# Optimization experiments

Hardware: AMD Instinct MI355X
Metric: run time of the kernel (lower is better)

## Reference

```python
import jax, jax.numpy as jnp
import numpy as np

B, L, D, N = 16, 512, 768, 8192


def setup_inputs() -> dict:
    key = jax.random.key(0)
    k = jax.random.split(key, 5)
    return {
        "y": jax.random.normal(k[0], (B, L, D), dtype=jnp.float32),
        "Wy_w": jax.random.normal(k[1], (D, D), dtype=jnp.float32) * 0.02,
        "Wy_b": jnp.zeros((D,), dtype=jnp.float32),
        "Wz_w": jax.random.normal(k[2], (D, D), dtype=jnp.float32) * 0.02,
        "Wz_b": jnp.zeros((D,), dtype=jnp.float32),
        "dic_z": jax.random.normal(k[3], (N, D), dtype=jnp.float32),
        "prior": jax.random.uniform(k[4], (N,), dtype=jnp.float32),
    }


def reference(y, Wy_w, Wy_b, Wz_w, Wz_b, dic_z, prior):
    # y: [B,L,D]; dic_z: [N,D]; prior: [N]
    d = y.shape[-1]
    qy = jnp.einsum('bld,ed->ble', y, Wy_w) + Wy_b          # Wy(y): [B,L,D]
    kz = jnp.einsum('nd,ed->ne', dic_z, Wz_w) + Wz_b        # Wz(dic_z): [N,D]
    scores = jnp.einsum('bld,nd->bln', qy, kz) / jnp.sqrt(jnp.float32(d))
    attn = jax.nn.softmax(scores, axis=-1)                   # [B,L,N]
    # z[b,l,d] = sum_n prior[n] * attn[b,l,n] * dic_z[n,d]
    # == (attn * prior) @ dic_z, avoiding the [L,N,D] intermediate.
    z = jnp.einsum('bln,nd->bld', attn * prior, dic_z)       # [B,L,D]
    return z
```

## Files before the change

### kernel.cpp

```cpp
#include <hip/hip_runtime.h>
#include <stdint.h>

#define M_ 8192
#define D_ 768
#define N_ 8192

typedef unsigned short u16;
typedef __attribute__((ext_vector_type(8))) unsigned short us8;
typedef __attribute__((ext_vector_type(8))) __bf16 bf16x8;
typedef __attribute__((ext_vector_type(4))) float f32x4;

__device__ __forceinline__ u16 f2bf(float f) {
  uint32_t u = __builtin_bit_cast(uint32_t, f);
  u += 0x7FFFu + ((u >> 16) & 1u);
  return (u16)(u >> 16);
}
__device__ __forceinline__ float bf2f(u16 u) {
  return __builtin_bit_cast(float, ((uint32_t)u) << 16);
}

__device__ __forceinline__ void gload_lds16(const void* g, void* l) {
  __builtin_amdgcn_global_load_lds(
      (__attribute__((address_space(1))) void*)g,
      (__attribute__((address_space(3))) void*)l, 16, 0, 0);
}

__global__ __launch_bounds__(256)
void k_cvt_bf16(const float* __restrict__ in, u16* __restrict__ out, int n4) {
  int stride = gridDim.x * blockDim.x;
  for (int i = blockIdx.x * blockDim.x + threadIdx.x; i < n4; i += stride) {
    float4 v = reinterpret_cast<const float4*>(in)[i];
    ushort4 o;
    o.x = f2bf(v.x); o.y = f2bf(v.y); o.z = f2bf(v.z); o.w = f2bf(v.w);
    reinterpret_cast<ushort4*>(out)[i] = o;
  }
}

__global__ __launch_bounds__(256)
void k_build_vt(const float* __restrict__ dic, const float* __restrict__ prior,
                u16* __restrict__ Vt) {
  __shared__ float t[32][33];
  const int n0 = blockIdx.x * 32, d0 = blockIdx.y * 32;
  const int tx = threadIdx.x, ty = threadIdx.y;
  #pragma unroll
  for (int i = ty; i < 32; i += 8)
    t[i][tx] = dic[(size_t)(n0 + i) * D_ + d0 + tx] * prior[n0 + i];
  __syncthreads();
  #pragma unroll
  for (int i = ty; i < 32; i += 8)
    Vt[(size_t)(d0 + i) * N_ + n0 + tx] = f2bf(t[tx][i]);
}

template<int EP>
__global__ __launch_bounds__(512, 2)
void k_gemm8(const u16* __restrict__ A, const u16* __restrict__ Bm,
             u16* __restrict__ Cb, float* __restrict__ Cf, float scale,
             long ldk, int K, int Ncols, int nbx, int tps, long partStride) {
  extern __shared__ u16 ldsu[];
  const int tid = threadIdx.x;
  const int lane = tid & 63, wid = tid >> 6;
  const int wr = wid >> 2, wc = wid & 3;
  const int L15 = lane & 15, L7 = lane & 7, g = lane >> 4;

  const int nwg = gridDim.x;
  const int bid = blockIdx.x;
  const int wg = ((nwg & 7) == 0) ? ((bid & 7) * (nwg >> 3) + (bid >> 3)) : bid;
  const int s = wg / tps;
  const int r = wg % tps;
  const int bx = r % nbx, by = r / nbx;
  const long m0 = (long)by * 256;
  const long n0 = (long)bx * 256;
  const int NT = K >> 6;

  int aBase[2], bBase[2];
  #pragma unroll
  for (int ks = 0; ks < 2; ++ks) {
    const int slot = (((ks * 4 + g) ^ L7) << 3);
    aBase[ks] = wr * 8192 + L15 * 64 + slot;
    bBase[ks] = 16384 + (wc >> 1) * 8192 + (wc & 1) * 4096 + L15 * 64 + slot;
  }

  const int rowoff = wid * 8 + (lane >> 3);
  const int colsw = ((lane & 7) ^ (lane >> 3)) << 3;
  const u16* Ag = A + m0 * ldk + (long)s * K;
  const u16* Bg = Bm + n0 * ldk + (long)s * K;
  u16* ldsW = ldsu + tid * 8;

  auto g1 = [&](int t, int mat, int r0) {
    if (t >= NT) return;
    const u16* src = (mat ? Bg : Ag) + (size_t)(r0 + rowoff) * ldk
                     + (size_t)t * 64 + colsw;
    gload_lds16(src, ldsW + (t & 1) * 32768 + mat * 16384 + (r0 >> 6) * 512 * 8);
  };

#define RD_B()                                                              \
  _Pragma("unroll") for (int j = 0; j < 4; ++j)                             \
    _Pragma("unroll") for (int ks = 0; ks < 2; ++ks)                        \
      bfr[j][ks] = __builtin_bit_cast(bf16x8,                               \
          *reinterpret_cast<const us8*>(&ldsu[bufOff + bBase[ks] + j * 1024]));
#define RD_A(q)                                                             \
  _Pragma("unroll") for (int t = 0; t < 2; ++t)                             \
    _Pragma("unroll") for (int ks = 0; ks < 2; ++ks)                        \
      afr[t][ks] = __builtin_bit_cast(bf16x8,                               \
          *reinterpret_cast<const us8*>(                                    \
              &ldsu[bufOff + aBase[ks] + (2 * (q) + t) * 1024]));
#define LGKM0()                                                             \
  asm volatile("s_waitcnt lgkmcnt(0)" ::: "memory");                        \
  __builtin_amdgcn_sched_barrier(0);
#define MM(p)                                                               \
  __builtin_amdgcn_s_setprio(1);                                            \
  _Pragma("unroll") for (int t = 0; t < 2; ++t)                             \
    _Pragma("unroll") for (int j = 0; j < 4; ++j)                           \
      _Pragma("unroll") for (int ks = 0; ks < 2; ++ks)                      \
        acc[2 * (p) + t][j] = __builtin_amdgcn_mfma_f32_16x16x32_bf16(      \
            afr[t][ks], bfr[j][ks], acc[2 * (p) + t][j], 0, 0, 0);          \
  __builtin_amdgcn_s_setprio(0);

  g1(0, 1, 0); g1(0, 1, 64); g1(0, 1, 128); g1(0, 1, 192);
  g1(0, 0, 0); g1(0, 0, 128); g1(0, 0, 64); g1(0, 0, 192);
  g1(1, 1, 0); g1(1, 1, 64);
  g1(1, 1, 128); g1(1, 1, 192);
  g1(1, 0, 0); g1(1, 0, 128);
  asm volatile("s_waitcnt vmcnt(6)" ::: "memory");
  __builtin_amdgcn_s_barrier();

  f32x4 acc[8][4] = {};

  for (int k = 0; k < NT; ++k) {
    const int bufOff = (k & 1) * 32768;
    bf16x8 bfr[4][2];

    {
      bf16x8 afr[2][2];
      g1(k + 1, 0, 64); g1(k + 1, 0, 192);
      RD_B(); RD_A(0);
      asm volatile("s_waitcnt lgkmcnt(8)" ::: "memory");
      __builtin_amdgcn_s_barrier();
      LGKM0();
      MM(0);
    }
    {
      bf16x8 afr[2][2];
      RD_A(1);
      g1(k + 2, 1, 0); g1(k + 2, 1, 64);
      __builtin_amdgcn_s_barrier();
      LGKM0();
      MM(1);
    }
    {
      bf16x8 afr[2][2];
      RD_A(2);
      g1(k + 2, 1, 128); g1(k + 2, 1, 192);
      __builtin_amdgcn_s_barrier();
      LGKM0();
      MM(2);
    }
    {
      bf16x8 afr[2][2];
      RD_A(3);
      g1(k + 2, 0, 0); g1(k + 2, 0, 128);
      if (k < NT - 2) asm volatile("s_waitcnt vmcnt(6)" ::: "memory");
      else            asm volatile("s_waitcnt vmcnt(0)" ::: "memory");
      __builtin_amdgcn_s_barrier();
      LGKM0();
      MM(3);
    }
  }
#undef RD_B
#undef RD_A
#undef LGKM0
#undef MM

  if (EP == 0) {
    __builtin_amdgcn_s_barrier();
    float* lsum = reinterpret_cast<float*>(ldsu);
    #pragma unroll
    for (int i = 0; i < 8; ++i) {
      #pragma unroll
      for (int q = 0; q < 4; ++q) {
        const int rl = wr * 128 + i * 16 + g * 4 + q;
        const long row = m0 + rl;
        float rsum = 0.f;
        #pragma unroll
        for (int j = 0; j < 4; ++j) {
          float v = __expf(acc[i][j][q] * scale);
          rsum += v;
          Cb[row * (long)Ncols + n0 + wc * 64 + j * 16 + L15] = f2bf(v);
        }
        lsum[rl * 68 + wc * 16 + L15] = rsum;
      }
    }
    __builtin_amdgcn_s_barrier();
    {
      const int rl = tid >> 1, half = tid & 1;
      const float4* rp =
          reinterpret_cast<const float4*>(&lsum[rl * 68 + half * 32]);
      float s4 = 0.f;
      #pragma unroll
      for (int c = 0; c < 8; ++c) {
        float4 v = rp[c];
        s4 += (v.x + v.y) + (v.z + v.w);
      }
      s4 += __shfl_xor(s4, 1);
      if (half == 0) atomicAdd(&Cf[m0 + rl], s4);
    }
  } else {
    #pragma unroll
    for (int i = 0; i < 8; ++i)
      #pragma unroll
      for (int j = 0; j < 4; ++j)
        #pragma unroll
        for (int q = 0; q < 4; ++q) {
          long row = m0 + wr * 128 + i * 16 + g * 4 + q;
          long col = n0 + wc * 64 + j * 16 + L15;
          Cf[(long)s * partStride + row * (long)Ncols + col] = acc[i][j][q];
        }
  }
}

template<int EP>
__global__ __launch_bounds__(256, 2)
void k_gemm_nt(const u16* __restrict__ A, const u16* __restrict__ Bm,
               float* __restrict__ Cf, u16* __restrict__ Cb,
               const float* __restrict__ bias, const float* __restrict__ rowsum,
               float scale, int N, long K) {
  __shared__ u16 Al[128 * 64];
  __shared__ u16 Bl[128 * 64];
  const int tid = threadIdx.x;
  const int lane = tid & 63;
  const int wave = tid >> 6;
  const int wr = wave >> 1, wc = wave & 1;
  const int L15 = lane & 15, L7 = lane & 7, g = lane >> 4;
  const long m0 = (long)blockIdx.y * 128;
  const long n0 = (long)blockIdx.x * 128;

  f32x4 acc[4][4] = {};

  const int colsw = ((tid & 7) ^ ((tid >> 3) & 7)) * 8;
  const u16* gA = A + (m0 + (tid >> 3)) * K + colsw;
  const u16* gB = Bm + (n0 + (tid >> 3)) * K + colsw;
  const int aslot = ((g) ^ L7) * 8;

  for (long kt = 0; kt < K; kt += 64) {
    __syncthreads();
    #pragma unroll
    for (int r = 0; r < 4; ++r) {
      gload_lds16(gA + (size_t)(r * 32) * K + kt, &Al[r * 2048 + tid * 8]);
      gload_lds16(gB + (size_t)(r * 32) * K + kt, &Bl[r * 2048 + tid * 8]);
    }
    __syncthreads();
    #pragma unroll
    for (int ks = 0; ks < 2; ++ks) {
      const int slot = ((ks * 4 + g) ^ L7) * 8;
      bf16x8 av[4], bv[4];
      #pragma unroll
      for (int i = 0; i < 4; ++i) {
        av[i] = __builtin_bit_cast(bf16x8, *reinterpret_cast<const us8*>(
            &Al[(wr * 64 + i * 16 + L15) * 64 + slot]));
        bv[i] = __builtin_bit_cast(bf16x8, *reinterpret_cast<const us8*>(
            &Bl[(wc * 64 + i * 16 + L15) * 64 + slot]));
      }
      #pragma unroll
      for (int i = 0; i < 4; ++i)
        #pragma unroll
        for (int j = 0; j < 4; ++j)
          acc[i][j] = __builtin_amdgcn_mfma_f32_16x16x32_bf16(av[i], bv[j], acc[i][j], 0, 0, 0);
    }
  }
  (void)aslot;

  #pragma unroll
  for (int i = 0; i < 4; ++i) {
    #pragma unroll
    for (int q = 0; q < 4; ++q) {
      long row = m0 + wr * 64 + i * 16 + g * 4 + q;
      float inv;
      if (EP == 3) inv = 1.0f / rowsum[row];
      #pragma unroll
      for (int j = 0; j < 4; ++j) {
        long col = n0 + wc * 64 + j * 16 + L15;
        float v = acc[i][j][q];
        if (EP == 1) Cb[row * N + col] = f2bf(v + bias[col]);
        else         Cf[row * N + col] = v * inv;
      }
    }
  }
  (void)scale;
}

extern "C" void kernel_launch(void* const* d_in, const int* in_sizes, int n_in,
                              void* d_out, int out_size, void* d_ws, size_t ws_size,
                              hipStream_t stream) {
  (void)in_sizes; (void)n_in; (void)out_size;
  const float* y     = (const float*)d_in[0];
  const float* Wy_w  = (const float*)d_in[1];
  const float* Wy_b  = (const float*)d_in[2];
  const float* Wz_w  = (const float*)d_in[3];
  const float* Wz_b  = (const float*)d_in[4];
  const float* dic   = (const float*)d_in[5];
  const float* prior = (const float*)d_in[6];
  float* out = (float*)d_out;

  hipFuncSetAttribute(reinterpret_cast<const void*>(&k_gemm8<0>),
                      hipFuncAttributeMaxDynamicSharedMemorySize, 131072);

  char* base = (char*)d_ws;
  size_t off = 0;
  auto alloc = [&](size_t bytes) -> char* {
    char* p = base + off;
    off = (off + bytes + 255) & ~(size_t)255;
    return p;
  };
  u16*  Yb   = (u16*)alloc((size_t)M_ * D_ * 2);
  u16*  Db   = (u16*)alloc((size_t)N_ * D_ * 2);
  u16*  Wyb  = (u16*)alloc((size_t)D_ * D_ * 2);
  u16*  Wzb  = (u16*)alloc((size_t)D_ * D_ * 2);
  u16*  Qb   = (u16*)alloc((size_t)M_ * D_ * 2);
  u16*  Kb   = (u16*)alloc((size_t)N_ * D_ * 2);
  u16*  Vt   = (u16*)alloc((size_t)D_ * N_ * 2);
  float* rowsum = (float*)alloc((size_t)M_ * 4);
  size_t fixed = off;
  int Mc = M_;
  while (Mc > 256 && fixed + (size_t)Mc * N_ * 2 > ws_size) Mc >>= 1;
  u16* Sc = (u16*)alloc((size_t)Mc * N_ * 2);

  hipMemsetAsync(rowsum, 0, (size_t)M_ * 4, stream);

  auto cvt = [&](const float* src, u16* dst, size_t n) {
    int n4 = (int)(n / 4);
    int blocks = (n4 + 255) / 256;
    if (blocks > 2048) blocks = 2048;
    hipLaunchKernelGGL(k_cvt_bf16, dim3(blocks), dim3(256), 0, stream, src, dst, n4);
  };
  cvt(y,    Yb,  (size_t)M_ * D_);
  cvt(dic,  Db,  (size_t)N_ * D_);
  cvt(Wy_w, Wyb, (size_t)D_ * D_);
  cvt(Wz_w, Wzb, (size_t)D_ * D_);

  hipLaunchKernelGGL(k_build_vt, dim3(N_ / 32, D_ / 32), dim3(32, 8), 0, stream,
                     dic, prior, Vt);

  hipLaunchKernelGGL(HIP_KERNEL_NAME(k_gemm_nt<1>), dim3(D_ / 128, M_ / 128), dim3(256), 0, stream,
                     Yb, Wyb, (float*)nullptr, Qb, Wy_b, (const float*)nullptr, 0.f, D_, (long)D_);
  hipLaunchKernelGGL(HIP_KERNEL_NAME(k_gemm_nt<1>), dim3(D_ / 128, N_ / 128), dim3(256), 0, stream,
                     Db, Wzb, (float*)nullptr, Kb, Wz_b, (const float*)nullptr, 0.f, D_, (long)D_);

  const float scale = 0.036084391824351615f;
  for (int mc = 0; mc < M_; mc += Mc) {
    {
      const int nbx = N_ / 256, nby = Mc / 256;
      hipLaunchKernelGGL(HIP_KERNEL_NAME(k_gemm8<0>), dim3(nbx * nby), dim3(512), 131072, stream,
                         Qb + (size_t)mc * D_, Kb, Sc, rowsum + mc, scale,
                         (long)D_, D_, N_, nbx, nbx * nby, 0L);
    }
    hipLaunchKernelGGL(HIP_KERNEL_NAME(k_gemm_nt<3>), dim3(D_ / 128, Mc / 128), dim3(256), 0, stream,
                       Sc, Vt, out + (size_t)mc * D_, (u16*)nullptr,
                       (const float*)nullptr, rowsum + mc, 0.f, D_, (long)N_);
  }
}
```

Before: 328.4 us.

## Add software-pipelined PV GEMM kernel and fuse dictionary bf16 conversion into Vt build

```diff
diff --git a/kernel.cpp b/kernel.cpp
--- a/kernel.cpp
+++ b/kernel.cpp
@@ -14,9 +14,6 @@
   uint32_t u = __builtin_bit_cast(uint32_t, f);
   u += 0x7FFFu + ((u >> 16) & 1u);
   return (u16)(u >> 16);
-}
-__device__ __forceinline__ float bf2f(u16 u) {
-  return __builtin_bit_cast(float, ((uint32_t)u) << 16);
 }
 
 __device__ __forceinline__ void gload_lds16(const void* g, void* l) {
@@ -37,14 +34,32 @@
 }
 
 __global__ __launch_bounds__(256)
+void k_cvt2(const float* __restrict__ a, const float* __restrict__ b,
+            u16* __restrict__ da, u16* __restrict__ db, int n4each) {
+  int stride = gridDim.x * blockDim.x;
+  for (int i = blockIdx.x * blockDim.x + threadIdx.x; i < 2 * n4each; i += stride) {
+    const float* s = (i < n4each) ? a : b;
+    u16* d = (i < n4each) ? da : db;
+    int j = (i < n4each) ? i : i - n4each;
+    float4 v = reinterpret_cast<const float4*>(s)[j];
+    ushort4 o;
+    o.x = f2bf(v.x); o.y = f2bf(v.y); o.z = f2bf(v.z); o.w = f2bf(v.w);
+    reinterpret_cast<ushort4*>(d)[j] = o;
+  }
+}
+
+__global__ __launch_bounds__(256)
 void k_build_vt(const float* __restrict__ dic, const float* __restrict__ prior,
-                u16* __restrict__ Vt) {
+                u16* __restrict__ Db, u16* __restrict__ Vt) {
   __shared__ float t[32][33];
   const int n0 = blockIdx.x * 32, d0 = blockIdx.y * 32;
   const int tx = threadIdx.x, ty = threadIdx.y;
   #pragma unroll
-  for (int i = ty; i < 32; i += 8)
-    t[i][tx] = dic[(size_t)(n0 + i) * D_ + d0 + tx] * prior[n0 + i];
+  for (int i = ty; i < 32; i += 8) {
+    float v = dic[(size_t)(n0 + i) * D_ + d0 + tx];
+    Db[(size_t)(n0 + i) * D_ + d0 + tx] = f2bf(v);
+    t[i][tx] = v * prior[n0 + i];
+  }
   __syncthreads();
   #pragma unroll
   for (int i = ty; i < 32; i += 8)
@@ -130,40 +145,32 @@
     const int bufOff = (k & 1) * 32768;
     bf16x8 bfr[4][2];
 
-    {
-      bf16x8 afr[2][2];
+    { bf16x8 afr[2][2];
       g1(k + 1, 0, 64); g1(k + 1, 0, 192);
       RD_B(); RD_A(0);
       asm volatile("s_waitcnt lgkmcnt(8)" ::: "memory");
       __builtin_amdgcn_s_barrier();
-      LGKM0();
-      MM(0);
-    }
-    {
-      bf16x8 afr[2][2];
+      LGKM0(); MM(0);
+    }
+    { bf16x8 afr[2][2];
       RD_A(1);
       g1(k + 2, 1, 0); g1(k + 2, 1, 64);
       __builtin_amdgcn_s_barrier();
-      LGKM0();
-      MM(1);
-    }
-    {
-      bf16x8 afr[2][2];
+      LGKM0(); MM(1);
+    }
+    { bf16x8 afr[2][2];
       RD_A(2);
       g1(k + 2, 1, 128); g1(k + 2, 1, 192);
       __builtin_amdgcn_s_barrier();
-      LGKM0();
-      MM(2);
-    }
-    {
-      bf16x8 afr[2][2];
+      LGKM0(); MM(2);
+    }
+    { bf16x8 afr[2][2];
       RD_A(3);
       g1(k + 2, 0, 0); g1(k + 2, 0, 128);
       if (k < NT - 2) asm volatile("s_waitcnt vmcnt(6)" ::: "memory");
       else            asm volatile("s_waitcnt vmcnt(0)" ::: "memory");
       __builtin_amdgcn_s_barrier();
-      LGKM0();
-      MM(3);
+      LGKM0(); MM(3);
     }
   }
 #undef RD_B
@@ -215,6 +222,128 @@
           long col = n0 + wc * 64 + j * 16 + L15;
           Cf[(long)s * partStride + row * (long)Ncols + col] = acc[i][j][q];
         }
+  }
+}
+
+__global__ __launch_bounds__(256, 2)
+void k_pv128(const u16* __restrict__ A, const u16* __restrict__ Bm,
+             const float* __restrict__ rowsum, float* __restrict__ out,
+             int nbx, long ldk, int K) {
+  extern __shared__ u16 ldsu[];
+  const int tid = threadIdx.x;
+  const int lane = tid & 63, wid = tid >> 6;
+  const int wr = wid >> 1, wc = wid & 1;
+  const int L15 = lane & 15, L7 = lane & 7, g = lane >> 4;
+
+  const int nwg = gridDim.x, bid = blockIdx.x;
+  const int wg = ((nwg & 7) == 0) ? ((bid & 7) * (nwg >> 3) + (bid >> 3)) : bid;
+  const int bx = wg % nbx, by = wg / nbx;
+  const long m0 = (long)by * 128, n0 = (long)bx * 128;
+  const int NT = K >> 6;
+
+  int aBase[2], bBase[2];
+  #pragma unroll
+  for (int ks = 0; ks < 2; ++ks) {
+    const int slot = (((ks * 4 + g) ^ L7) << 3);
+    aBase[ks] = (wr * 64 + L15) * 64 + slot;
+    bBase[ks] = 8192 + (wc * 64 + L15) * 64 + slot;
+  }
+
+  const int rowoff = tid >> 3;
+  const int colsw = ((tid & 7) ^ ((tid >> 3) & 7)) << 3;
+  const u16* Ag = A + m0 * ldk;
+  const u16* Bg = Bm + n0 * ldk;
+  u16* ldsW = ldsu + tid * 8;
+
+  auto g1 = [&](int t, int mat, int r0) {
+    if (t >= NT) return;
+    const u16* src = (mat ? Bg : Ag) + (size_t)(r0 + rowoff) * ldk
+                     + (size_t)t * 64 + colsw;
+    gload_lds16(src, ldsW + (t & 1) * 16384 + mat * 8192 + r0 * 64);
+  };
+
+#define PLGKM0()                                                            \
+  asm volatile("s_waitcnt lgkmcnt(0)" ::: "memory");                        \
+  __builtin_amdgcn_sched_barrier(0);
+#define PMM(p)                                                              \
+  __builtin_amdgcn_s_setprio(1);                                            \
+  _Pragma("unroll") for (int j = 0; j < 4; ++j)                             \
+    _Pragma("unroll") for (int ks = 0; ks < 2; ++ks)                        \
+      acc[p][j] = __builtin_amdgcn_mfma_f32_16x16x32_bf16(                  \
+          afr[ks], bfr[j][ks], acc[p][j], 0, 0, 0);                         \
+  __builtin_amdgcn_s_setprio(0);
+#define PRD_A(q)                                                            \
+  _Pragma("unroll") for (int ks = 0; ks < 2; ++ks)                          \
+    afr[ks] = __builtin_bit_cast(bf16x8,                                    \
+        *reinterpret_cast<const us8*>(&ldsu[bufOff + aBase[ks] + (q) * 1024]));
+
+  g1(0, 1, 0); g1(0, 1, 32); g1(0, 1, 64); g1(0, 1, 96);
+  g1(0, 0, 0); g1(0, 0, 32); g1(0, 0, 64); g1(0, 0, 96);
+  g1(1, 1, 0); g1(1, 1, 32); g1(1, 1, 64); g1(1, 1, 96);
+  g1(1, 0, 0); g1(1, 0, 32);
+  asm volatile("s_waitcnt vmcnt(6)" ::: "memory");
+  __builtin_amdgcn_s_barrier();
+
+  f32x4 acc[4][4] = {};
+
+  for (int k = 0; k < NT; ++k) {
+    const int bufOff = (k & 1) * 16384;
+    bf16x8 bfr[4][2];
+
+    {
+      bf16x8 afr[2];
+      g1(k + 1, 0, 64); g1(k + 1, 0, 96);
+      #pragma unroll
+      for (int j = 0; j < 4; ++j)
+        #pragma unroll
+        for (int ks = 0; ks < 2; ++ks)
+          bfr[j][ks] = __builtin_bit_cast(bf16x8,
+              *reinterpret_cast<const us8*>(&ldsu[bufOff + bBase[ks] + j * 1024]));
+      PRD_A(0);
+      asm volatile("s_waitcnt lgkmcnt(8)" ::: "memory");
+      __builtin_amdgcn_s_barrier();
+      PLGKM0(); PMM(0);
+    }
+    {
+      bf16x8 afr[2];
+      PRD_A(1);
+      g1(k + 2, 1, 0); g1(k + 2, 1, 32);
+      __builtin_amdgcn_s_barrier();
+      PLGKM0(); PMM(1);
+    }
+    {
+      bf16x8 afr[2];
+      PRD_A(2);
+      g1(k + 2, 1, 64); g1(k + 2, 1, 96);
+      __builtin_amdgcn_s_barrier();
+      PLGKM0(); PMM(2);
+    }
+    {
+      bf16x8 afr[2];
+      PRD_A(3);
+      g1(k + 2, 0, 0); g1(k + 2, 0, 32);
+      if (k < NT - 2) asm volatile("s_waitcnt vmcnt(6)" ::: "memory");
+      else            asm volatile("s_waitcnt vmcnt(0)" ::: "memory");
+      __builtin_amdgcn_s_barrier();
+      PLGKM0(); PMM(3);
+    }
+  }
+#undef PLGKM0
+#undef PMM
+#undef PRD_A
+
+  #pragma unroll
+  for (int i = 0; i < 4; ++i) {
+    #pragma unroll
+    for (int q = 0; q < 4; ++q) {
+      long row = m0 + wr * 64 + i * 16 + g * 4 + q;
+      float inv = 1.0f / rowsum[row];
+      #pragma unroll
+      for (int j = 0; j < 4; ++j) {
+        long col = n0 + wc * 64 + j * 16 + L15;
+        out[row * D_ + col] = acc[i][j][q] * inv;
+      }
+    }
   }
 }
 
@@ -239,7 +368,6 @@
   const int colsw = ((tid & 7) ^ ((tid >> 3) & 7)) * 8;
   const u16* gA = A + (m0 + (tid >> 3)) * K + colsw;
   const u16* gB = Bm + (n0 + (tid >> 3)) * K + colsw;
-  const int aslot = ((g) ^ L7) * 8;
 
   for (long kt = 0; kt < K; kt += 64) {
     __syncthreads();
@@ -267,7 +395,6 @@
           acc[i][j] = __builtin_amdgcn_mfma_f32_16x16x32_bf16(av[i], bv[j], acc[i][j], 0, 0, 0);
     }
   }
-  (void)aslot;
 
   #pragma unroll
   for (int i = 0; i < 4; ++i) {
@@ -303,6 +430,8 @@
 
   hipFuncSetAttribute(reinterpret_cast<const void*>(&k_gemm8<0>),
                       hipFuncAttributeMaxDynamicSharedMemorySize, 131072);
+  hipFuncSetAttribute(reinterpret_cast<const void*>(&k_pv128),
+                      hipFuncAttributeMaxDynamicSharedMemorySize, 65536);
 
   char* base = (char*)d_ws;
   size_t off = 0;
@@ -326,19 +455,22 @@
 
   hipMemsetAsync(rowsum, 0, (size_t)M_ * 4, stream);
 
-  auto cvt = [&](const float* src, u16* dst, size_t n) {
-    int n4 = (int)(n / 4);
+  {
+    int n4 = M_ * D_ / 4;
     int blocks = (n4 + 255) / 256;
     if (blocks > 2048) blocks = 2048;
-    hipLaunchKernelGGL(k_cvt_bf16, dim3(blocks), dim3(256), 0, stream, src, dst, n4);
-  };
-  cvt(y,    Yb,  (size_t)M_ * D_);
-  cvt(dic,  Db,  (size_t)N_ * D_);
-  cvt(Wy_w, Wyb, (size_t)D_ * D_);
-  cvt(Wz_w, Wzb, (size_t)D_ * D_);
+    hipLaunchKernelGGL(k_cvt_bf16, dim3(blocks), dim3(256), 0, stream, y, Yb, n4);
+  }
+  {
+    int n4e = D_ * D_ / 4;
+    int blocks = (2 * n4e + 255) / 256;
+    if (blocks > 2048) blocks = 2048;
+    hipLaunchKernelGGL(k_cvt2, dim3(blocks), dim3(256), 0, stream,
+                       Wy_w, Wz_w, Wyb, Wzb, n4e);
+  }
 
   hipLaunchKernelGGL(k_build_vt, dim3(N_ / 32, D_ / 32), dim3(32, 8), 0, stream,
-                     dic, prior, Vt);
+                     dic, prior, Db, Vt);
 
   hipLaunchKernelGGL(HIP_KERNEL_NAME(k_gemm_nt<1>), dim3(D_ / 128, M_ / 128), dim3(256), 0, stream,
                      Yb, Wyb, (float*)nullptr, Qb, Wy_b, (const float*)nullptr, 0.f, D_, (long)D_);
@@ -353,8 +485,11 @@
                          Qb + (size_t)mc * D_, Kb, Sc, rowsum + mc, scale,
                          (long)D_, D_, N_, nbx, nbx * nby, 0L);
     }
-    hipLaunchKernelGGL(HIP_KERNEL_NAME(k_gemm_nt<3>), dim3(D_ / 128, Mc / 128), dim3(256), 0, stream,
-                       Sc, Vt, out + (size_t)mc * D_, (u16*)nullptr,
-                       (const float*)nullptr, rowsum + mc, 0.f, D_, (long)N_);
-  }
-}
+    {
+      const int nbx = D_ / 128, nby = Mc / 128;
+      hipLaunchKernelGGL(k_pv128, dim3(nbx * nby), dim3(256), 65536, stream,
+                         Sc, Vt, rowsum + mc, out + (size_t)mc * D_,
+                         nbx, (long)N_, N_);
+    }
+  }
+}
```

Result: faster. 295.8 us (-9.9%).
